# Kernel tuning notes

Hardware: AMD Instinct MI355X
Metric: run time of the kernel (lower is better)

The kernel has to match this reference:

```python
import jax, jax.numpy as jnp
import numpy as np

D = 1024          # d_input_feature
GCN_OUTS = [1024, 512, 256]
DEC_OUTS = [512, 1024, 1024]  # reversed[1:] + [d_input_feature]
EPS = 1e-3        # keras LayerNormalization default epsilon


def _ln(x, gamma, beta):
    m = jnp.mean(x, axis=-1, keepdims=True)
    v = jnp.mean(jnp.square(x - m), axis=-1, keepdims=True)
    return gamma * (x - m) * jax.lax.rsqrt(v + EPS) + beta


def _gcn(x, A, W, b, act):
    # message passing with dense adjacency: act((A @ x) @ W + b)
    h = jnp.einsum('bij,bjd->bid', A, x)
    return act(h @ W + b)


def setup_inputs() -> dict:
    key = jax.random.key(0)
    ks = jax.random.split(key, 40)
    B, DG, DC, NTT = 16384, 772, 100, 128
    inp = {
        't_1': jax.random.randint(ks[0], (B,), 0, NTT),
        'g_1': jax.random.normal(ks[1], (B, DG), jnp.float32),
        'c_1': jax.random.normal(ks[2], (B, DC), jnp.float32),
        'A_1': jax.random.uniform(ks[3], (B, 3, 3), jnp.float32),
        't_2': jax.random.randint(ks[4], (B,), 0, NTT),
        'g_2': jax.random.normal(ks[5], (B, DG), jnp.float32),
        'c_2': jax.random.normal(ks[6], (B, DC), jnp.float32),
        'A_2': jax.random.uniform(ks[7], (B, 3, 3), jnp.float32),
        'embed': jax.random.normal(ks[8], (NTT, D), jnp.float32) * 0.02,
        'Wt': jax.random.normal(ks[9], (D, D), jnp.float32) / np.sqrt(D),
        'bt': jnp.zeros((D,), jnp.float32),
        'Wg': jax.random.normal(ks[10], (DG, D), jnp.float32) / np.sqrt(DG),
        'bg': jnp.zeros((D,), jnp.float32),
        'Wc': jax.random.normal(ks[11], (DC, D), jnp.float32) / np.sqrt(DC),
        'bc': jnp.zeros((D,), jnp.float32),
        'ln_t_g': jnp.ones((D,), jnp.float32), 'ln_t_b': jnp.zeros((D,), jnp.float32),
        'ln_g_g': jnp.ones((D,), jnp.float32), 'ln_g_b': jnp.zeros((D,), jnp.float32),
        'ln_c_g': jnp.ones((D,), jnp.float32), 'ln_c_b': jnp.zeros((D,), jnp.float32),
    }
    d_in = D
    for i, d_out in enumerate(GCN_OUTS):
        inp[f'enc_W{i}'] = jax.random.normal(ks[12 + i], (d_in, d_out), jnp.float32) / np.sqrt(d_in)
        inp[f'enc_b{i}'] = jnp.zeros((d_out,), jnp.float32)
        d_in = d_out
    for i, d_out in enumerate(DEC_OUTS):
        inp[f'dec_W{i}'] = jax.random.normal(ks[20 + i], (d_in, d_out), jnp.float32) / np.sqrt(d_in)
        inp[f'dec_b{i}'] = jnp.zeros((d_out,), jnp.float32)
        d_in = d_out
    return inp


def _branch(t, g, c, embed, Wt, bt, Wg, bg, Wc, bc,
            ln_t_g, ln_t_b, ln_g_g, ln_g_b, ln_c_g, ln_c_b):
    te = embed[t]                               # [B, D]
    te = jax.nn.relu(te @ Wt + bt)
    ge = jax.nn.relu(g @ Wg + bg)
    ce = jax.nn.relu(c @ Wc + bc)
    te = _ln(te, ln_t_g, ln_t_b)
    ge = _ln(ge, ln_g_g, ln_g_b)
    ce = _ln(ce, ln_c_g, ln_c_b)
    return jnp.stack([te, ge, ce], axis=1)      # [B, 3, D]


def _encoder(X, A, enc):
    x = X
    for W, b in enc:
        x = _gcn(x, A, W, b, jax.nn.relu)
    return x


def _decoder(Z, A, dec):
    x = Z
    for W, b in dec:
        x = _gcn(x, A, W, b, jax.nn.silu)       # swish
    return x


def reference(t_1, g_1, c_1, A_1, t_2, g_2, c_2, A_2,
              embed, Wt, bt, Wg, bg, Wc, bc,
              ln_t_g, ln_t_b, ln_g_g, ln_g_b, ln_c_g, ln_c_b,
              enc_W0, enc_b0, enc_W1, enc_b1, enc_W2, enc_b2,
              dec_W0, dec_b0, dec_W1, dec_b1, dec_W2, dec_b2):
    enc = [(enc_W0, enc_b0), (enc_W1, enc_b1), (enc_W2, enc_b2)]
    dec = [(dec_W0, dec_b0), (dec_W1, dec_b1), (dec_W2, dec_b2)]
    bargs = (embed, Wt, bt, Wg, bg, Wc, bc,
             ln_t_g, ln_t_b, ln_g_g, ln_g_b, ln_c_g, ln_c_b)

    X_1 = _branch(t_1, g_1, c_1, *bargs)
    X_2 = _branch(t_2, g_2, c_2, *bargs)
    Z_1 = _encoder(X_1, A_1, enc)
    Z_2 = _encoder(X_2, A_2, enc)
    Z_loss = jnp.square(Z_1 - Z_2)              # [B, 3, 256]

    # GAE reconstruction path (recomputes X per the original code)
    X_h_1 = _decoder(Z_1, A_1, dec)
    X_h_2 = _decoder(Z_2, A_2, dec)
    X_loss = (jnp.square(X_1 - X_h_1) + jnp.square(X_2 - X_h_2)) / 2.0  # [B, 3, D]
    return Z_loss, X_loss
```

## Files before the change

kernel.cpp:

```cpp
#include <hip/hip_runtime.h>


typedef __attribute__((ext_vector_type(8))) short s16x8;
typedef __attribute__((ext_vector_type(4))) short s16x4;
typedef __attribute__((ext_vector_type(4))) float f32x4;

#define DEV static __device__ __forceinline__

DEV float b2f(ushort u) { return __builtin_bit_cast(float, (unsigned)u << 16); }
DEV ushort f2b(float f) {
  unsigned x = __builtin_bit_cast(unsigned, f);
  unsigned r = x + 0x7fffu + ((x >> 16) & 1u);
  return (ushort)(r >> 16);
}

typedef const __attribute__((address_space(1))) void* gas_ptr;
typedef __attribute__((address_space(3))) void* las_ptr;

template<int ACT>
__global__ __launch_bounds__(512, 2) void gemm256(
    const ushort* __restrict__ A, const ushort* __restrict__ BT,
    const float* __restrict__ bias, ushort* __restrict__ C,
    int M, int N, int K)
{
  __shared__ __align__(16) ushort ldsbuf[65536];
  char* Lb = (char*)ldsbuf;

  const int tid = threadIdx.x, lane = tid & 63, w = tid >> 6;
  const int wm = w >> 2, wn = w & 3;

  const int gx  = gridDim.x;
  const int nwg = gx * gridDim.y;
  const int wid = blockIdx.y * gx + blockIdx.x;
  const int q   = nwg >> 3;
  const int Lw  = (wid & 7) * q + (wid >> 3);
  const int bn  = Lw % gx;
  const int bm  = Lw / gx;

  const ushort* Abase = A  + (size_t)bm * 256 * K;
  const ushort* Bbase = BT + (size_t)bn * 256 * K;
  const int T = K >> 6;

  const int srow = w * 8 + (lane >> 3);
  const int scol = (((lane & 7) ^ (lane >> 3)) << 3);

#define STAGE(buf, m, half, Gb, k0)                                          \
  {                                                                          \
    _Pragma("unroll") for (int _j = 0; _j < 2; ++_j) {                       \
      const ushort* _src = (Gb) + (size_t)((half)*128 + _j*64 + srow) * K    \
                           + (k0) + scol;                                    \
      ushort* _dst = (ushort*)(Lb + ((buf)*2 + (m)) * 32768                  \
                               + ((half)*128 + _j*64 + w*8) * 128);          \
      __builtin_amdgcn_global_load_lds((gas_ptr)_src, (las_ptr)_dst, 16,0,0);\
    }                                                                        \
  }

  const int lr = lane & 15, lk = lane >> 4;

#define READ_A(dst, c, mh)                                                   \
  _Pragma("unroll") for (int _i = 0; _i < 4; ++_i)                           \
    _Pragma("unroll") for (int _kk = 0; _kk < 2; ++_kk) {                    \
      const int _r   = (mh)*128 + wm*64 + _i*16 + lr;                        \
      const int _cbb = _kk*64 + lk*16;                                       \
      dst[_i][_kk] = *(const s16x8*)(Lb + ((c)*2 + 0)*32768 + _r*128         \
                                     + (_cbb ^ ((_r & 7) << 4)));            \
    }
#define READ_B(dst, c, nh)                                                   \
  _Pragma("unroll") for (int _p = 0; _p < 2; ++_p)                           \
    _Pragma("unroll") for (int _kk = 0; _kk < 2; ++_kk) {                    \
      const int _r   = (nh)*128 + wn*32 + _p*16 + lr;                        \
      const int _cbb = _kk*64 + lk*16;                                       \
      dst[_p][_kk] = *(const s16x8*)(Lb + ((c)*2 + 1)*32768 + _r*128         \
                                     + (_cbb ^ ((_r & 7) << 4)));            \
    }

#define MFMA_Q(mh, nh)                                                       \
  _Pragma("unroll") for (int _i = 0; _i < 4; ++_i)                           \
    _Pragma("unroll") for (int _p = 0; _p < 2; ++_p)                         \
      _Pragma("unroll") for (int _kk = 0; _kk < 2; ++_kk)                    \
        acc[(mh)*4 + _i][(nh)*2 + _p] =                                      \
            __builtin_amdgcn_mfma_f32_16x16x32_bf16(                         \
                af[_i][_kk], bf[_p][_kk], acc[(mh)*4 + _i][(nh)*2 + _p],     \
                0, 0, 0);

#define MIDBAR  do { __builtin_amdgcn_s_barrier();                           \
                     asm volatile("s_waitcnt lgkmcnt(0)" ::: "memory");      \
                     __builtin_amdgcn_sched_barrier(0);                      \
                     __builtin_amdgcn_s_setprio(1); } while (0)
#define ENDBAR  do { __builtin_amdgcn_s_setprio(0);                          \
                     __builtin_amdgcn_s_barrier(); } while (0)

  f32x4 acc[8][4];
  #pragma unroll
  for (int i = 0; i < 8; ++i)
    #pragma unroll
    for (int j = 0; j < 4; ++j) acc[i][j] = f32x4{0.f, 0.f, 0.f, 0.f};

  STAGE(0, 0, 0, Abase, 0);
  STAGE(0, 1, 0, Bbase, 0);
  STAGE(0, 1, 1, Bbase, 0);
  STAGE(0, 0, 1, Abase, 0);
  STAGE(1, 0, 0, Abase, 64);
  STAGE(1, 1, 1, Bbase, 64);
  STAGE(1, 0, 1, Abase, 64);
  asm volatile("s_waitcnt vmcnt(6)" ::: "memory");
  __builtin_amdgcn_s_barrier();

  for (int t = 0; t < T; ++t) {
    const int cbuf = t & 1, nbuf = cbuf ^ 1;
    const int k1 = ((t + 1 < T) ? t + 1 : t + 1 - T) * 64;
    const int k2 = ((t + 2 < T) ? t + 2 : t + 2 - T) * 64;
    s16x8 af[4][2], bf[2][2];
    READ_A(af, cbuf, 0);
    READ_B(bf, cbuf, 0);
    STAGE(nbuf, 1, 0, Bbase, k1);
    asm volatile("s_waitcnt lgkmcnt(8)" ::: "memory");
    MIDBAR; MFMA_Q(0, 0); ENDBAR;
    READ_B(bf, cbuf, 1);
    STAGE(cbuf, 0, 0, Abase, k2);
    MIDBAR; MFMA_Q(0, 1); ENDBAR;
    READ_A(af, cbuf, 1);
    STAGE(cbuf, 1, 1, Bbase, k2);
    MIDBAR; MFMA_Q(1, 1); ENDBAR;
    READ_B(bf, cbuf, 0);
    STAGE(cbuf, 0, 1, Abase, k2);
    MIDBAR; MFMA_Q(1, 0);
    __builtin_amdgcn_s_setprio(0);
    asm volatile("s_waitcnt vmcnt(6)" ::: "memory");
    __builtin_amdgcn_s_barrier();
  }

  const int row0 = bm * 256, col0 = bn * 256;
  #pragma unroll
  for (int mi = 0; mi < 8; ++mi) {
    const int row = row0 + (mi >> 2) * 128 + wm * 64 + (mi & 3) * 16 + lk * 4;
    #pragma unroll
    for (int ni = 0; ni < 4; ++ni) {
      const int col = col0 + (ni >> 1) * 128 + wn * 32 + (ni & 1) * 16 + lr;
      const float bv = bias[col];
      #pragma unroll
      for (int r = 0; r < 4; ++r) {
        float v = acc[mi][ni][r] + bv;
        if (ACT == 0) v = fmaxf(v, 0.f);
        else          v = v / (1.f + __expf(-v));
        C[(size_t)(row + r) * N + col] = f2b(v);
      }
    }
  }
#undef STAGE
#undef READ_A
#undef READ_B
#undef MFMA_Q
#undef MIDBAR
#undef ENDBAR
}

template<int ACT>
__global__ __launch_bounds__(256, 2) void gemm128(
    const ushort* __restrict__ A, const ushort* __restrict__ BT,
    const float* __restrict__ bias, ushort* __restrict__ C,
    int M, int N, int K)
{
  __shared__ __align__(16) ushort lds[32768];
  char* Lb = (char*)lds;

  const int tid = threadIdx.x, lane = tid & 63;
  const int w = tid >> 6;
  const int wm = w >> 1, wn = w & 1;

  const int gx  = gridDim.x;
  const int nwg = gx * gridDim.y;
  const int wid = blockIdx.y * gx + blockIdx.x;
  const int q   = nwg >> 3;
  const int Lw  = (wid & 7) * q + (wid >> 3);
  const int bn  = Lw % gx;
  const int bm  = Lw / gx;

  const ushort* Abase = A  + (size_t)bm * 128 * K;
  const ushort* Bbase = BT + (size_t)bn * 128 * K;
  const int T = K >> 6;

  const int srow = tid >> 3;
  const int scol = (((tid & 7) ^ (srow & 7)) << 3);

#define STAGE128(buf, k0)                                                    \
  {                                                                          \
    _Pragma("unroll") for (int _j = 0; _j < 4; ++_j)                         \
      __builtin_amdgcn_global_load_lds(                                      \
          (gas_ptr)(Abase + (size_t)(_j * 32 + srow) * K + (k0) + scol),     \
          (las_ptr)(Lb + (buf) + _j * 4096 + tid * 16), 16, 0, 0);           \
    _Pragma("unroll") for (int _j = 0; _j < 4; ++_j)                         \
      __builtin_amdgcn_global_load_lds(                                      \
          (gas_ptr)(Bbase + (size_t)(_j * 32 + srow) * K + (k0) + scol),     \
          (las_ptr)(Lb + (buf) + 16384 + _j * 4096 + tid * 16), 16, 0, 0);   \
  }

  const int lr = lane & 15, lk = lane >> 4;

  f32x4 acc[4][4];
  #pragma unroll
  for (int f = 0; f < 4; ++f)
    #pragma unroll
    for (int p = 0; p < 4; ++p) acc[f][p] = f32x4{0.f, 0.f, 0.f, 0.f};

  STAGE128(0, 0);
  __syncthreads();

  for (int t = 0; t < T; ++t) {
    const int cb = (t & 1) << 15, nb = cb ^ 32768;
    if (t + 1 < T) STAGE128(nb, (t + 1) << 6);

    s16x8 af[4][2], bf[4][2];
    #pragma unroll
    for (int f = 0; f < 4; ++f)
      #pragma unroll
      for (int kk = 0; kk < 2; ++kk) {
        const int r = wm * 64 + f * 16 + lr;
        af[f][kk] = *(const s16x8*)(Lb + cb + r * 128
                                    + ((kk * 64 + lk * 16) ^ ((r & 7) << 4)));
      }
    #pragma unroll
    for (int p = 0; p < 4; ++p)
      #pragma unroll
      for (int kk = 0; kk < 2; ++kk) {
        const int r = wn * 64 + p * 16 + lr;
        bf[p][kk] = *(const s16x8*)(Lb + cb + 16384 + r * 128
                                    + ((kk * 64 + lk * 16) ^ ((r & 7) << 4)));
      }
    #pragma unroll
    for (int f = 0; f < 4; ++f)
      #pragma unroll
      for (int p = 0; p < 4; ++p)
        #pragma unroll
        for (int kk = 0; kk < 2; ++kk)
          acc[f][p] = __builtin_amdgcn_mfma_f32_16x16x32_bf16(
              af[f][kk], bf[p][kk], acc[f][p], 0, 0, 0);

    __syncthreads();
  }

  const int row0 = bm * 128 + wm * 64;
  const int col0 = bn * 128 + wn * 64;
  #pragma unroll
  for (int f = 0; f < 4; ++f) {
    const int row = row0 + f * 16 + lk * 4;
    #pragma unroll
    for (int p = 0; p < 4; ++p) {
      const int col = col0 + p * 16 + lr;
      const float bv = bias[col];
      #pragma unroll
      for (int r = 0; r < 4; ++r) {
        float v = acc[f][p][r] + bv;
        if (ACT == 0) v = fmaxf(v, 0.f);
        else          v = v / (1.f + __expf(-v));
        C[(size_t)(row + r) * N + col] = f2b(v);
      }
    }
  }
#undef STAGE128
}

__global__ void trans_conv(const float* __restrict__ W, ushort* __restrict__ WT,
                           int K, int N, int Kpad)
{
  __shared__ float tile[32][33];
  const int n0 = blockIdx.x * 32, k0 = blockIdx.y * 32;
  const int tx = threadIdx.x, ty = threadIdx.y;
  #pragma unroll
  for (int r = 0; r < 4; r++) {
    const int k = k0 + ty + r * 8;
    tile[ty + r * 8][tx] = (k < K) ? W[(size_t)k * N + n0 + tx] : 0.f;
  }
  __syncthreads();
  #pragma unroll
  for (int r = 0; r < 4; r++) {
    const int n = n0 + ty + r * 8;
    WT[(size_t)n * Kpad + k0 + tx] = f2b(tile[tx][ty + r * 8]);
  }
}

__global__ void conv_pad(const float* __restrict__ in, ushort* __restrict__ out,
                         int R, int Cin, int Cpad)
{
  const int gid = blockIdx.x * 256 + threadIdx.x;
  if (gid >= R * Cpad) return;
  const int r = gid / Cpad, c = gid - r * Cpad;
  out[gid] = (c < Cin) ? f2b(in[(size_t)r * Cin + c]) : (ushort)0;
}

DEV void ln_row(const ushort* __restrict__ in, const float* __restrict__ gamma,
                const float* __restrict__ beta, ushort* __restrict__ outp,
                int tid, float* red)
{
  s16x4 v = *(const s16x4*)&in[tid * 4];
  const float x0 = b2f((ushort)v[0]), x1 = b2f((ushort)v[1]);
  const float x2 = b2f((ushort)v[2]), x3 = b2f((ushort)v[3]);
  float s = x0 + x1 + x2 + x3;
  float qq = x0 * x0 + x1 * x1 + x2 * x2 + x3 * x3;
  #pragma unroll
  for (int o = 32; o > 0; o >>= 1) { s += __shfl_down(s, o); qq += __shfl_down(qq, o); }
  const int wv = tid >> 6, lane = tid & 63;
  __syncthreads();
  if (lane == 0) { red[wv] = s; red[4 + wv] = qq; }
  __syncthreads();
  s  = red[0] + red[1] + red[2] + red[3];
  qq = red[4] + red[5] + red[6] + red[7];
  const float m   = s * (1.f / 1024.f);
  const float var = qq * (1.f / 1024.f) - m * m;
  const float rs  = rsqrtf(var + 1e-3f);
  const int c = tid * 4;
  s16x4 o;
  o[0] = (short)f2b(gamma[c + 0] * ((x0 - m) * rs) + beta[c + 0]);
  o[1] = (short)f2b(gamma[c + 1] * ((x1 - m) * rs) + beta[c + 1]);
  o[2] = (short)f2b(gamma[c + 2] * ((x2 - m) * rs) + beta[c + 2]);
  o[3] = (short)f2b(gamma[c + 3] * ((x3 - m) * rs) + beta[c + 3]);
  *(s16x4*)&outp[c] = o;
}

__global__ void ln_te(const ushort* __restrict__ in, const float* __restrict__ g,
                      const float* __restrict__ b, ushort* __restrict__ out)
{
  __shared__ float red[8];
  ln_row(in + (size_t)blockIdx.x * 1024, g, b,
         out + (size_t)blockIdx.x * 1024, threadIdx.x, red);
}

__global__ void assembleX(const int* __restrict__ ta, const int* __restrict__ tb,
                          int split, const ushort* __restrict__ tetab,
                          const ushort* __restrict__ ge, const ushort* __restrict__ ce,
                          const float* __restrict__ gG, const float* __restrict__ gB,
                          const float* __restrict__ cG, const float* __restrict__ cB,
                          ushort* __restrict__ X)
{
  __shared__ float red[8];
  const int b = blockIdx.x, tid = threadIdx.x;
  const int tt = (b < split) ? ta[b] : tb[b - split];
  *(s16x4*)&X[(size_t)b * 3072 + tid * 4] =
      *(const s16x4*)&tetab[(size_t)tt * 1024 + tid * 4];
  ln_row(ge + (size_t)b * 1024, gG, gB, X + (size_t)b * 3072 + 1024, tid, red);
  ln_row(ce + (size_t)b * 1024, cG, cB, X + (size_t)b * 3072 + 2048, tid, red);
}

__global__ void mix3(const ushort* __restrict__ x,
                     const float* __restrict__ Aa, const float* __restrict__ Ab2,
                     int split, ushort* __restrict__ out, int d, int lg, int nB)
{
  const int gid = blockIdx.x * 256 + threadIdx.x;
  const int b = gid >> lg;
  if (b >= nB) return;
  const int c8 = (gid & ((1 << lg) - 1)) << 3;
  const ushort* xb = x   + (size_t)b * 3 * d + c8;
  ushort*       ob = out + (size_t)b * 3 * d + c8;
  s16x8 x0 = *(const s16x8*)xb;
  s16x8 x1 = *(const s16x8*)(xb + d);
  s16x8 x2 = *(const s16x8*)(xb + 2 * d);
  float f0[8], f1[8], f2[8];
  #pragma unroll
  for (int e = 0; e < 8; e++) {
    f0[e] = b2f((ushort)x0[e]); f1[e] = b2f((ushort)x1[e]); f2[e] = b2f((ushort)x2[e]);
  }
  const float* Ab = (b < split) ? (Aa + (size_t)b * 9)
                                : (Ab2 + (size_t)(b - split) * 9);
  #pragma unroll
  for (int j = 0; j < 3; j++) {
    const float a0 = Ab[j * 3], a1 = Ab[j * 3 + 1], a2 = Ab[j * 3 + 2];
    s16x8 o;
    #pragma unroll
    for (int e = 0; e < 8; e++)
      o[e] = (short)f2b(a0 * f0[e] + a1 * f1[e] + a2 * f2[e]);
    *(s16x8*)(ob + j * d) = o;
  }
}

__global__ void zloss_k(const ushort* __restrict__ z1, const ushort* __restrict__ z2,
                        float* __restrict__ out, int n8)
{
  const int gid = blockIdx.x * 256 + threadIdx.x;
  if (gid >= n8) return;
  const size_t i = (size_t)gid * 8;
  s16x8 a = *(const s16x8*)&z1[i];
  s16x8 b = *(const s16x8*)&z2[i];
  f32x4 o0, o1;
  #pragma unroll
  for (int e = 0; e < 4; e++) {
    float d0 = b2f((ushort)a[e]) - b2f((ushort)b[e]);
    float d1 = b2f((ushort)a[e + 4]) - b2f((ushort)b[e + 4]);
    o0[e] = d0 * d0; o1[e] = d1 * d1;
  }
  *(f32x4*)&out[i] = o0; *(f32x4*)&out[i + 4] = o1;
}

__global__ void xloss2_k(const ushort* __restrict__ X1, const ushort* __restrict__ Xh1,
                         const ushort* __restrict__ X2, const ushort* __restrict__ Xh2,
                         float* __restrict__ out, int n8)
{
  const int gid = blockIdx.x * 256 + threadIdx.x;
  if (gid >= n8) return;
  const size_t i = (size_t)gid * 8;
  s16x8 a1 = *(const s16x8*)&X1[i];
  s16x8 h1 = *(const s16x8*)&Xh1[i];
  s16x8 a2 = *(const s16x8*)&X2[i];
  s16x8 h2 = *(const s16x8*)&Xh2[i];
  f32x4 o0, o1;
  #pragma unroll
  for (int e = 0; e < 4; e++) {
    float d1a = b2f((ushort)a1[e])     - b2f((ushort)h1[e]);
    float d2a = b2f((ushort)a2[e])     - b2f((ushort)h2[e]);
    float d1b = b2f((ushort)a1[e + 4]) - b2f((ushort)h1[e + 4]);
    float d2b = b2f((ushort)a2[e + 4]) - b2f((ushort)h2[e + 4]);
    o0[e] = 0.5f * (d1a * d1a + d2a * d2a);
    o1[e] = 0.5f * (d1b * d1b + d2b * d2b);
  }
  *(f32x4*)&out[i] = o0; *(f32x4*)&out[i + 4] = o1;
}

extern "C" void kernel_launch(void* const* d_in, const int* in_sizes, int n_in,
                              void* d_out, int out_size, void* d_ws, size_t ws_size,
                              hipStream_t stream)
{
  const int B = 16384, S = 3 * B;
  const int*   t1 = (const int*)d_in[0];
  const float* g1 = (const float*)d_in[1];
  const float* c1 = (const float*)d_in[2];
  const float* A1 = (const float*)d_in[3];
  const int*   t2 = (const int*)d_in[4];
  const float* g2 = (const float*)d_in[5];
  const float* c2 = (const float*)d_in[6];
  const float* A2 = (const float*)d_in[7];
  const float* embed = (const float*)d_in[8];
  const float* Wt = (const float*)d_in[9];  const float* bt = (const float*)d_in[10];
  const float* Wg = (const float*)d_in[11]; const float* bg = (const float*)d_in[12];
  const float* Wc = (const float*)d_in[13]; const float* bc = (const float*)d_in[14];
  const float* lntg = (const float*)d_in[15]; const float* lntb = (const float*)d_in[16];
  const float* lngg = (const float*)d_in[17]; const float* lngb = (const float*)d_in[18];
  const float* lncg = (const float*)d_in[19]; const float* lncb = (const float*)d_in[20];
  const float* eW0 = (const float*)d_in[21]; const float* eb0 = (const float*)d_in[22];
  const float* eW1 = (const float*)d_in[23]; const float* eb1 = (const float*)d_in[24];
  const float* eW2 = (const float*)d_in[25]; const float* eb2 = (const float*)d_in[26];
  const float* dW0 = (const float*)d_in[27]; const float* db0 = (const float*)d_in[28];
  const float* dW1 = (const float*)d_in[29]; const float* db1 = (const float*)d_in[30];
  const float* dW2 = (const float*)d_in[31]; const float* db2 = (const float*)d_in[32];
  float* out = (float*)d_out;
  (void)in_sizes; (void)n_in; (void)out_size;

  char* ws = (char*)d_ws; size_t off = 0;
  auto alloc = [&](size_t bytes) -> void* {
    void* p = ws + off; off += (bytes + 255) & ~(size_t)255; return p;
  };
  ushort* WtT  = (ushort*)alloc((size_t)1024 * 1024 * 2);
  ushort* WgT  = (ushort*)alloc((size_t)1024 * 896 * 2);
  ushort* WcT  = (ushort*)alloc((size_t)1024 * 128 * 2);
  ushort* E0T  = (ushort*)alloc((size_t)1024 * 1024 * 2);
  ushort* E1T  = (ushort*)alloc((size_t)512 * 1024 * 2);
  ushort* E2T  = (ushort*)alloc((size_t)256 * 512 * 2);
  ushort* D0T  = (ushort*)alloc((size_t)512 * 256 * 2);
  ushort* D1T  = (ushort*)alloc((size_t)1024 * 512 * 2);
  ushort* D2T  = (ushort*)alloc((size_t)1024 * 1024 * 2);
  ushort* embB = (ushort*)alloc((size_t)128 * 1024 * 2);
  ushort* teraw= (ushort*)alloc((size_t)128 * 1024 * 2);
  ushort* tetab= (ushort*)alloc((size_t)128 * 1024 * 2);
  const size_t woff = off;

  ushort* G  = (ushort*)alloc((size_t)2 * B * 896 * 2);
  ushort* Cc = (ushort*)alloc((size_t)2 * B * 128 * 2);
  ushort* Z  = (ushort*)alloc((size_t)2 * S * 256 * 2);
  ushort* Xs = (ushort*)alloc((size_t)2 * S * 1024 * 2);
  ushort* b0 = (ushort*)alloc((size_t)2 * S * 1024 * 2);
  ushort* b1 = (ushort*)alloc((size_t)2 * S * 1024 * 2);
  const bool merged = (off <= ws_size);

  ushort *fG[2], *fC[2], *fZ[2], *fX[2], *fb0, *fb1, *fxh;
  if (!merged) {
    off = woff;
    fG[0] = (ushort*)alloc((size_t)B * 896 * 2);
    fG[1] = (ushort*)alloc((size_t)B * 896 * 2);
    fC[0] = (ushort*)alloc((size_t)B * 128 * 2);
    fC[1] = (ushort*)alloc((size_t)B * 128 * 2);
    fZ[0] = (ushort*)alloc((size_t)S * 256 * 2);
    fZ[1] = (ushort*)alloc((size_t)S * 256 * 2);
    fX[0] = (ushort*)alloc((size_t)S * 1024 * 2);
    fX[1] = (ushort*)alloc((size_t)S * 1024 * 2);
    fb0   = (ushort*)alloc((size_t)S * 1024 * 2);
    fb1   = (ushort*)alloc((size_t)S * 1024 * 2);
    fxh   = (ushort*)alloc((size_t)S * 1024 * 2);
  }

  const dim3 TB(32, 8);
  trans_conv<<<dim3(32, 32), TB, 0, stream>>>(Wt,  WtT, 1024, 1024, 1024);
  trans_conv<<<dim3(32, 28), TB, 0, stream>>>(Wg,  WgT,  772, 1024,  896);
  trans_conv<<<dim3(32,  4), TB, 0, stream>>>(Wc,  WcT,  100, 1024,  128);
  trans_conv<<<dim3(32, 32), TB, 0, stream>>>(eW0, E0T, 1024, 1024, 1024);
  trans_conv<<<dim3(16, 32), TB, 0, stream>>>(eW1, E1T, 1024,  512, 1024);
  trans_conv<<<dim3( 8, 16), TB, 0, stream>>>(eW2, E2T,  512,  256,  512);
  trans_conv<<<dim3(16,  8), TB, 0, stream>>>(dW0, D0T,  256,  512,  256);
  trans_conv<<<dim3(32, 16), TB, 0, stream>>>(dW1, D1T,  512, 1024,  512);
  trans_conv<<<dim3(32, 32), TB, 0, stream>>>(dW2, D2T, 1024, 1024, 1024);
  conv_pad<<<512, 256, 0, stream>>>(embed, embB, 128, 1024, 1024);
  gemm128<0><<<dim3(8, 1), 256, 0, stream>>>(embB, WtT, bt, teraw, 128, 1024, 1024);
  ln_te<<<128, 256, 0, stream>>>(teraw, lntg, lntb, tetab);

  const size_t ZLEN = (size_t)S * 256;
  const int n8x = S * 1024 / 8;

  auto pipeline = [&](ushort* Gp, ushort* Cp, const int* ta, const int* tb,
                      const float* Aa, const float* Ab2, int split, int nS,
                      ushort* Xp, ushort* p0, ushort* p1, ushort* Zp, ushort* xh) {
    const int Ms = nS * 3;
    gemm256<0><<<dim3(4, nS / 256), 512, 0, stream>>>(Gp, WgT, bg, p0, nS, 1024, 896);
    gemm128<0><<<dim3(8, nS / 128), 256, 0, stream>>>(Cp, WcT, bc, p1, nS, 1024, 128);
    assembleX<<<nS, 256, 0, stream>>>(ta, tb, split, tetab, p0, p1,
                                      lngg, lngb, lncg, lncb, Xp);
    mix3<<<(nS << 7) / 256, 256, 0, stream>>>(Xp, Aa, Ab2, split, p0, 1024, 7, nS);
    gemm256<0><<<dim3(4, Ms / 256), 512, 0, stream>>>(p0, E0T, eb0, p1, Ms, 1024, 1024);
    mix3<<<(nS << 7) / 256, 256, 0, stream>>>(p1, Aa, Ab2, split, p0, 1024, 7, nS);
    gemm256<0><<<dim3(2, Ms / 256), 512, 0, stream>>>(p0, E1T, eb1, p1, Ms, 512, 1024);
    mix3<<<(nS << 6) / 256, 256, 0, stream>>>(p1, Aa, Ab2, split, p0, 512, 6, nS);
    gemm128<0><<<dim3(2, Ms / 128), 256, 0, stream>>>(p0, E2T, eb2, Zp, Ms, 256, 512);
    mix3<<<(nS << 5) / 256, 256, 0, stream>>>(Zp, Aa, Ab2, split, p0, 256, 5, nS);
    gemm128<1><<<dim3(4, Ms / 128), 256, 0, stream>>>(p0, D0T, db0, p1, Ms, 512, 256);
    mix3<<<(nS << 6) / 256, 256, 0, stream>>>(p1, Aa, Ab2, split, p0, 512, 6, nS);
    gemm256<1><<<dim3(4, Ms / 256), 512, 0, stream>>>(p0, D1T, db1, p1, Ms, 1024, 512);
    mix3<<<(nS << 7) / 256, 256, 0, stream>>>(p1, Aa, Ab2, split, p0, 1024, 7, nS);
    gemm256<1><<<dim3(4, Ms / 256), 512, 0, stream>>>(p0, D2T, db2, xh, Ms, 1024, 1024);
  };

  if (merged) {
    conv_pad<<<(B * 896 + 255) / 256, 256, 0, stream>>>(g1, G, B, 772, 896);
    conv_pad<<<(B * 896 + 255) / 256, 256, 0, stream>>>(g2, G + (size_t)B * 896, B, 772, 896);
    conv_pad<<<B * 128 / 256, 256, 0, stream>>>(c1, Cc, B, 100, 128);
    conv_pad<<<B * 128 / 256, 256, 0, stream>>>(c2, Cc + (size_t)B * 128, B, 100, 128);
    pipeline(G, Cc, t1, t2, A1, A2, B, 2 * B, Xs, b0, b1, Z, b1);
    xloss2_k<<<n8x / 256, 256, 0, stream>>>(
        Xs, b1, Xs + (size_t)S * 1024, b1 + (size_t)S * 1024, out + ZLEN, n8x);
    zloss_k<<<(int)(ZLEN / 8 / 256), 256, 0, stream>>>(Z, Z + ZLEN, out, (int)(ZLEN / 8));
  } else {
    for (int br = 0; br < 2; ++br) {
      conv_pad<<<(B * 896 + 255) / 256, 256, 0, stream>>>(br ? g2 : g1, fG[br], B, 772, 896);
      conv_pad<<<B * 128 / 256, 256, 0, stream>>>(br ? c2 : c1, fC[br], B, 100, 128);
      const int*   t    = br ? t2 : t1;
      const float* Aadj = br ? A2 : A1;
      pipeline(fG[br], fC[br], t, t, Aadj, Aadj, B, B,
               fX[br], fb0, fb1, fZ[br], br ? fb1 : fxh);
    }
    xloss2_k<<<n8x / 256, 256, 0, stream>>>(fX[0], fxh, fX[1], fb1, out + ZLEN, n8x);
    zloss_k<<<(int)(ZLEN / 8 / 256), 256, 0, stream>>>(fZ[0], fZ[1], out, (int)(ZLEN / 8));
  }
}
```

Measured before the change: 1.487 ms.

## Fuse 3x3 adjacency mixing into GEMM A-operand load path

Removes the six standalone mix3 kernels and adds a gemm128m kernel that loads three node rows per output row, applies the per-sample 3x3 adjacency weights in registers, and writes the mixed bf16 tile into LDS before the MFMA loop. This avoids a full write and re-read of each layer's activations through global memory. In exchange, every GEMM now uses 128x128 tiles instead of the larger 256-tile variant for the big layers. The A operand also goes through register loads and VALU math instead of direct global-to-LDS copies, and each A element is re-read by the three row tiles that share a sample.

```diff
diff --git a/kernel.cpp b/kernel.cpp
--- a/kernel.cpp
+++ b/kernel.cpp
@@ -260,6 +260,143 @@
 #undef STAGE128
 }
 
+template<int ACT>
+__global__ __launch_bounds__(256, 2) void gemm128m(
+    const ushort* __restrict__ x,
+    const float* __restrict__ Aa, const float* __restrict__ Ab2, int split,
+    const ushort* __restrict__ BT, const float* __restrict__ bias,
+    ushort* __restrict__ C, int M, int N, int K)
+{
+  __shared__ __align__(16) ushort lds[32768];
+  char* Lb = (char*)lds;
+
+  const int tid = threadIdx.x, lane = tid & 63;
+  const int w = tid >> 6;
+  const int wm = w >> 1, wn = w & 1;
+
+  const int gx  = gridDim.x;
+  const int nwg = gx * gridDim.y;
+  const int wid = blockIdx.y * gx + blockIdx.x;
+  const int q   = nwg >> 3;
+  const int Lw  = (wid & 7) * q + (wid >> 3);
+  const int bn  = Lw % gx;
+  const int bm  = Lw / gx;
+
+  const ushort* Bbase = BT + (size_t)bn * 128 * K;
+  const int T = K >> 6;
+
+  const int srow  = tid >> 3;
+  const int lin8  = (tid & 7) * 8;
+  const int swz16 = ((tid & 7) ^ (srow & 7)) << 4;
+  const int swcol = ((tid & 7) ^ (srow & 7)) << 3;
+
+  const ushort* xrow[4];
+  float av[4][3];
+  #pragma unroll
+  for (int j = 0; j < 4; ++j) {
+    const int g = bm * 128 + j * 32 + srow;
+    const int b = g / 3;
+    const int i = g - 3 * b;
+    const float* ad = (b < split) ? (Aa + (size_t)b * 9 + i * 3)
+                                  : (Ab2 + (size_t)(b - split) * 9 + i * 3);
+    av[j][0] = ad[0]; av[j][1] = ad[1]; av[j][2] = ad[2];
+    xrow[j] = x + (size_t)(3 * b) * K + lin8;
+  }
+
+#define STAGEB_M(buf, k0)                                                    \
+  { _Pragma("unroll") for (int _j = 0; _j < 4; ++_j)                         \
+      __builtin_amdgcn_global_load_lds(                                      \
+          (gas_ptr)(Bbase + (size_t)(_j * 32 + srow) * K + (k0) + swcol),    \
+          (las_ptr)(Lb + (buf) + 16384 + _j * 4096 + tid * 16), 16, 0, 0); }
+
+  s16x8 xr[4][3];
+#define LOADX(k0)                                                            \
+  { _Pragma("unroll") for (int _j = 0; _j < 4; ++_j) {                       \
+      const ushort* _xb = xrow[_j] + (k0);                                   \
+      xr[_j][0] = *(const s16x8*)_xb;                                        \
+      xr[_j][1] = *(const s16x8*)(_xb + K);                                  \
+      xr[_j][2] = *(const s16x8*)(_xb + 2 * K); } }
+
+#define WRITEX(buf)                                                          \
+  { _Pragma("unroll") for (int _j = 0; _j < 4; ++_j) {                       \
+      s16x8 _o;                                                              \
+      _Pragma("unroll") for (int _e = 0; _e < 8; ++_e)                       \
+        _o[_e] = (short)f2b(av[_j][0] * b2f((ushort)xr[_j][0][_e])           \
+                          + av[_j][1] * b2f((ushort)xr[_j][1][_e])           \
+                          + av[_j][2] * b2f((ushort)xr[_j][2][_e]));         \
+      *(s16x8*)(Lb + (buf) + _j * 4096 + srow * 128 + swz16) = _o; } }
+
+  const int lr = lane & 15, lk = lane >> 4;
+
+  f32x4 acc[4][4];
+  #pragma unroll
+  for (int f = 0; f < 4; ++f)
+    #pragma unroll
+    for (int p = 0; p < 4; ++p) acc[f][p] = f32x4{0.f, 0.f, 0.f, 0.f};
+
+  LOADX(0);
+  STAGEB_M(0, 0);
+  WRITEX(0);
+  __syncthreads();
+
+  for (int t = 0; t < T; ++t) {
+    const int cb = (t & 1) << 15, nb = cb ^ 32768;
+    const bool hn = (t + 1 < T);
+    if (hn) { STAGEB_M(nb, (t + 1) << 6); LOADX((t + 1) << 6); }
+
+    s16x8 af[4][2], bf[4][2];
+    #pragma unroll
+    for (int f = 0; f < 4; ++f)
+      #pragma unroll
+      for (int kk = 0; kk < 2; ++kk) {
+        const int r = wm * 64 + f * 16 + lr;
+        af[f][kk] = *(const s16x8*)(Lb + cb + r * 128
+                                    + ((kk * 64 + lk * 16) ^ ((r & 7) << 4)));
+      }
+    #pragma unroll
+    for (int p = 0; p < 4; ++p)
+      #pragma unroll
+      for (int kk = 0; kk < 2; ++kk) {
+        const int r = wn * 64 + p * 16 + lr;
+        bf[p][kk] = *(const s16x8*)(Lb + cb + 16384 + r * 128
+                                    + ((kk * 64 + lk * 16) ^ ((r & 7) << 4)));
+      }
+    #pragma unroll
+    for (int f = 0; f < 4; ++f)
+      #pragma unroll
+      for (int p = 0; p < 4; ++p)
+        #pragma unroll
+        for (int kk = 0; kk < 2; ++kk)
+          acc[f][p] = __builtin_amdgcn_mfma_f32_16x16x32_bf16(
+              af[f][kk], bf[p][kk], acc[f][p], 0, 0, 0);
+
+    if (hn) WRITEX(nb);
+    __syncthreads();
+  }
+
+  const int row0 = bm * 128 + wm * 64;
+  const int col0 = bn * 128 + wn * 64;
+  #pragma unroll
+  for (int f = 0; f < 4; ++f) {
+    const int row = row0 + f * 16 + lk * 4;
+    #pragma unroll
+    for (int p = 0; p < 4; ++p) {
+      const int col = col0 + p * 16 + lr;
+      const float bv = bias[col];
+      #pragma unroll
+      for (int r = 0; r < 4; ++r) {
+        float v = acc[f][p][r] + bv;
+        if (ACT == 0) v = fmaxf(v, 0.f);
+        else          v = v / (1.f + __expf(-v));
+        C[(size_t)(row + r) * N + col] = f2b(v);
+      }
+    }
+  }
+#undef STAGEB_M
+#undef LOADX
+#undef WRITEX
+}
+
 __global__ void trans_conv(const float* __restrict__ W, ushort* __restrict__ WT,
                            int K, int N, int Kpad)
 {
@@ -339,37 +476,6 @@
       *(const s16x4*)&tetab[(size_t)tt * 1024 + tid * 4];
   ln_row(ge + (size_t)b * 1024, gG, gB, X + (size_t)b * 3072 + 1024, tid, red);
   ln_row(ce + (size_t)b * 1024, cG, cB, X + (size_t)b * 3072 + 2048, tid, red);
-}
-
-__global__ void mix3(const ushort* __restrict__ x,
-                     const float* __restrict__ Aa, const float* __restrict__ Ab2,
-                     int split, ushort* __restrict__ out, int d, int lg, int nB)
-{
-  const int gid = blockIdx.x * 256 + threadIdx.x;
-  const int b = gid >> lg;
-  if (b >= nB) return;
-  const int c8 = (gid & ((1 << lg) - 1)) << 3;
-  const ushort* xb = x   + (size_t)b * 3 * d + c8;
-  ushort*       ob = out + (size_t)b * 3 * d + c8;
-  s16x8 x0 = *(const s16x8*)xb;
-  s16x8 x1 = *(const s16x8*)(xb + d);
-  s16x8 x2 = *(const s16x8*)(xb + 2 * d);
-  float f0[8], f1[8], f2[8];
-  #pragma unroll
-  for (int e = 0; e < 8; e++) {
-    f0[e] = b2f((ushort)x0[e]); f1[e] = b2f((ushort)x1[e]); f2[e] = b2f((ushort)x2[e]);
-  }
-  const float* Ab = (b < split) ? (Aa + (size_t)b * 9)
-                                : (Ab2 + (size_t)(b - split) * 9);
-  #pragma unroll
-  for (int j = 0; j < 3; j++) {
-    const float a0 = Ab[j * 3], a1 = Ab[j * 3 + 1], a2 = Ab[j * 3 + 2];
-    s16x8 o;
-    #pragma unroll
-    for (int e = 0; e < 8; e++)
-      o[e] = (short)f2b(a0 * f0[e] + a1 * f1[e] + a2 * f2[e]);
-    *(s16x8*)(ob + j * d) = o;
-  }
 }
 
 __global__ void zloss_k(const ushort* __restrict__ z1, const ushort* __restrict__ z2,
@@ -510,18 +616,12 @@
     gemm128<0><<<dim3(8, nS / 128), 256, 0, stream>>>(Cp, WcT, bc, p1, nS, 1024, 128);
     assembleX<<<nS, 256, 0, stream>>>(ta, tb, split, tetab, p0, p1,
                                       lngg, lngb, lncg, lncb, Xp);
-    mix3<<<(nS << 7) / 256, 256, 0, stream>>>(Xp, Aa, Ab2, split, p0, 1024, 7, nS);
-    gemm256<0><<<dim3(4, Ms / 256), 512, 0, stream>>>(p0, E0T, eb0, p1, Ms, 1024, 1024);
-    mix3<<<(nS << 7) / 256, 256, 0, stream>>>(p1, Aa, Ab2, split, p0, 1024, 7, nS);
-    gemm256<0><<<dim3(2, Ms / 256), 512, 0, stream>>>(p0, E1T, eb1, p1, Ms, 512, 1024);
-    mix3<<<(nS << 6) / 256, 256, 0, stream>>>(p1, Aa, Ab2, split, p0, 512, 6, nS);
-    gemm128<0><<<dim3(2, Ms / 128), 256, 0, stream>>>(p0, E2T, eb2, Zp, Ms, 256, 512);
-    mix3<<<(nS << 5) / 256, 256, 0, stream>>>(Zp, Aa, Ab2, split, p0, 256, 5, nS);
-    gemm128<1><<<dim3(4, Ms / 128), 256, 0, stream>>>(p0, D0T, db0, p1, Ms, 512, 256);
-    mix3<<<(nS << 6) / 256, 256, 0, stream>>>(p1, Aa, Ab2, split, p0, 512, 6, nS);
-    gemm256<1><<<dim3(4, Ms / 256), 512, 0, stream>>>(p0, D1T, db1, p1, Ms, 1024, 512);
-    mix3<<<(nS << 7) / 256, 256, 0, stream>>>(p1, Aa, Ab2, split, p0, 1024, 7, nS);
-    gemm256<1><<<dim3(4, Ms / 256), 512, 0, stream>>>(p0, D2T, db2, xh, Ms, 1024, 1024);
+    gemm128m<0><<<dim3(8, Ms / 128), 256, 0, stream>>>(Xp, Aa, Ab2, split, E0T, eb0, p1, Ms, 1024, 1024);
+    gemm128m<0><<<dim3(4, Ms / 128), 256, 0, stream>>>(p1, Aa, Ab2, split, E1T, eb1, p0, Ms, 512, 1024);
+    gemm128m<0><<<dim3(2, Ms / 128), 256, 0, stream>>>(p0, Aa, Ab2, split, E2T, eb2, Zp, Ms, 256, 512);
+    gemm128m<1><<<dim3(4, Ms / 128), 256, 0, stream>>>(Zp, Aa, Ab2, split, D0T, db0, p1, Ms, 512, 256);
+    gemm128m<1><<<dim3(8, Ms / 128), 256, 0, stream>>>(p1, Aa, Ab2, split, D1T, db1, p0, Ms, 1024, 512);
+    gemm128m<1><<<dim3(8, Ms / 128), 256, 0, stream>>>(p0, Aa, Ab2, split, D2T, db2, xh, Ms, 1024, 1024);
   };
 
   if (merged) {
```

After: 1.860 ms. +25.1%, slower.

## Reorder encoder layers to apply weights before adjacency mix, batch prep kernels

Applied to the files above, without the earlier changes.

For encoder layers 1 and 2, the GEMM now runs first on the unmixed input with no bias or activation, and a new mixact kernel then applies the 3x3 adjacency mix, bias and ReLU. This uses associativity (A·X)·W = A·(X·W), so the mix works on the narrower output width (512 or 256) instead of the wider input. The nine weight-transpose launches are merged into one 3D-grid kernel, and the five input convert/pad launches into one grid-stride kernel, to cut launch overhead. Rounding to bf16 now happens at a different point, which slightly changes the numerics.

```diff
diff --git a/kernel.cpp b/kernel.cpp
--- a/kernel.cpp
+++ b/kernel.cpp
@@ -137,12 +137,12 @@
     #pragma unroll
     for (int ni = 0; ni < 4; ++ni) {
       const int col = col0 + (ni >> 1) * 128 + wn * 32 + (ni & 1) * 16 + lr;
-      const float bv = bias[col];
+      const float bv = (ACT == 2) ? 0.f : bias[col];
       #pragma unroll
       for (int r = 0; r < 4; ++r) {
         float v = acc[mi][ni][r] + bv;
-        if (ACT == 0) v = fmaxf(v, 0.f);
-        else          v = v / (1.f + __expf(-v));
+        if (ACT == 0)      v = fmaxf(v, 0.f);
+        else if (ACT == 1) v = v / (1.f + __expf(-v));
         C[(size_t)(row + r) * N + col] = f2b(v);
       }
     }
@@ -247,12 +247,12 @@
     #pragma unroll
     for (int p = 0; p < 4; ++p) {
       const int col = col0 + p * 16 + lr;
-      const float bv = bias[col];
+      const float bv = (ACT == 2) ? 0.f : bias[col];
       #pragma unroll
       for (int r = 0; r < 4; ++r) {
         float v = acc[f][p][r] + bv;
-        if (ACT == 0) v = fmaxf(v, 0.f);
-        else          v = v / (1.f + __expf(-v));
+        if (ACT == 0)      v = fmaxf(v, 0.f);
+        else if (ACT == 1) v = v / (1.f + __expf(-v));
         C[(size_t)(row + r) * N + col] = f2b(v);
       }
     }
@@ -260,32 +260,45 @@
 #undef STAGE128
 }
 
-__global__ void trans_conv(const float* __restrict__ W, ushort* __restrict__ WT,
-                           int K, int N, int Kpad)
+struct TP { const float* W; ushort* WT; int K, N, Kpad; };
+struct TP9 { TP t[9]; };
+
+__global__ void trans_all(TP9 ps)
 {
   __shared__ float tile[32][33];
+  const TP tp = ps.t[blockIdx.z];
   const int n0 = blockIdx.x * 32, k0 = blockIdx.y * 32;
+  if (n0 >= tp.N || k0 >= tp.Kpad) return;
   const int tx = threadIdx.x, ty = threadIdx.y;
   #pragma unroll
   for (int r = 0; r < 4; r++) {
     const int k = k0 + ty + r * 8;
-    tile[ty + r * 8][tx] = (k < K) ? W[(size_t)k * N + n0 + tx] : 0.f;
+    tile[ty + r * 8][tx] = (k < tp.K) ? tp.W[(size_t)k * tp.N + n0 + tx] : 0.f;
   }
   __syncthreads();
   #pragma unroll
   for (int r = 0; r < 4; r++) {
     const int n = n0 + ty + r * 8;
-    WT[(size_t)n * Kpad + k0 + tx] = f2b(tile[tx][ty + r * 8]);
-  }
-}
-
-__global__ void conv_pad(const float* __restrict__ in, ushort* __restrict__ out,
-                         int R, int Cin, int Cpad)
-{
-  const int gid = blockIdx.x * 256 + threadIdx.x;
-  if (gid >= R * Cpad) return;
-  const int r = gid / Cpad, c = gid - r * Cpad;
-  out[gid] = (c < Cin) ? f2b(in[(size_t)r * Cin + c]) : (ushort)0;
+    tp.WT[(size_t)n * tp.Kpad + k0 + tx] = f2b(tile[tx][ty + r * 8]);
+  }
+}
+
+struct CP { const float* in; ushort* out; int Cin, Cpad; size_t total; };
+struct CP5 { CP s[5]; size_t cum[5]; };
+
+__global__ void conv_all(CP5 ps, size_t grand)
+{
+  for (size_t gid = (size_t)blockIdx.x * 256 + threadIdx.x; gid < grand;
+       gid += (size_t)gridDim.x * 256) {
+    int si = 0;
+    #pragma unroll
+    for (int k = 1; k < 5; ++k) si += (gid >= ps.cum[k - 1]);
+    const CP sp = ps.s[si];
+    const size_t l = gid - (si ? ps.cum[si - 1] : 0);
+    const size_t r = l / sp.Cpad;
+    const int c = (int)(l - r * sp.Cpad);
+    sp.out[l] = (c < sp.Cin) ? f2b(sp.in[r * sp.Cin + c]) : (ushort)0;
+  }
 }
 
 DEV void ln_row(const ushort* __restrict__ in, const float* __restrict__ gamma,
@@ -368,6 +381,42 @@
     #pragma unroll
     for (int e = 0; e < 8; e++)
       o[e] = (short)f2b(a0 * f0[e] + a1 * f1[e] + a2 * f2[e]);
+    *(s16x8*)(ob + j * d) = o;
+  }
+}
+
+__global__ void mixact(const ushort* __restrict__ y,
+                       const float* __restrict__ Aa, const float* __restrict__ Ab2,
+                       int split, const float* __restrict__ bias,
+                       ushort* __restrict__ out, int d, int lg, int nB)
+{
+  const int gid = blockIdx.x * 256 + threadIdx.x;
+  const int b = gid >> lg;
+  if (b >= nB) return;
+  const int c8 = (gid & ((1 << lg) - 1)) << 3;
+  const ushort* yb = y   + (size_t)b * 3 * d + c8;
+  ushort*       ob = out + (size_t)b * 3 * d + c8;
+  s16x8 y0 = *(const s16x8*)yb;
+  s16x8 y1 = *(const s16x8*)(yb + d);
+  s16x8 y2 = *(const s16x8*)(yb + 2 * d);
+  f32x4 bv0 = *(const f32x4*)&bias[c8];
+  f32x4 bv1 = *(const f32x4*)&bias[c8 + 4];
+  float f0[8], f1[8], f2[8];
+  #pragma unroll
+  for (int e = 0; e < 8; e++) {
+    f0[e] = b2f((ushort)y0[e]); f1[e] = b2f((ushort)y1[e]); f2[e] = b2f((ushort)y2[e]);
+  }
+  const float* Ab = (b < split) ? (Aa + (size_t)b * 9)
+                                : (Ab2 + (size_t)(b - split) * 9);
+  #pragma unroll
+  for (int j = 0; j < 3; j++) {
+    const float a0 = Ab[j * 3], a1 = Ab[j * 3 + 1], a2 = Ab[j * 3 + 2];
+    s16x8 o;
+    #pragma unroll
+    for (int e = 0; e < 8; e++) {
+      const float bb = (e < 4) ? bv0[e] : bv1[e - 4];
+      o[e] = (short)f2b(fmaxf(a0 * f0[e] + a1 * f1[e] + a2 * f2[e] + bb, 0.f));
+    }
     *(s16x8*)(ob + j * d) = o;
   }
 }
@@ -485,17 +534,42 @@
     fxh   = (ushort*)alloc((size_t)S * 1024 * 2);
   }
 
-  const dim3 TB(32, 8);
-  trans_conv<<<dim3(32, 32), TB, 0, stream>>>(Wt,  WtT, 1024, 1024, 1024);
-  trans_conv<<<dim3(32, 28), TB, 0, stream>>>(Wg,  WgT,  772, 1024,  896);
-  trans_conv<<<dim3(32,  4), TB, 0, stream>>>(Wc,  WcT,  100, 1024,  128);
-  trans_conv<<<dim3(32, 32), TB, 0, stream>>>(eW0, E0T, 1024, 1024, 1024);
-  trans_conv<<<dim3(16, 32), TB, 0, stream>>>(eW1, E1T, 1024,  512, 1024);
-  trans_conv<<<dim3( 8, 16), TB, 0, stream>>>(eW2, E2T,  512,  256,  512);
-  trans_conv<<<dim3(16,  8), TB, 0, stream>>>(dW0, D0T,  256,  512,  256);
-  trans_conv<<<dim3(32, 16), TB, 0, stream>>>(dW1, D1T,  512, 1024,  512);
-  trans_conv<<<dim3(32, 32), TB, 0, stream>>>(dW2, D2T, 1024, 1024, 1024);
-  conv_pad<<<512, 256, 0, stream>>>(embed, embB, 128, 1024, 1024);
+  TP9 tp;
+  tp.t[0] = {Wt,  WtT, 1024, 1024, 1024};
+  tp.t[1] = {Wg,  WgT,  772, 1024,  896};
+  tp.t[2] = {Wc,  WcT,  100, 1024,  128};
+  tp.t[3] = {eW0, E0T, 1024, 1024, 1024};
+  tp.t[4] = {eW1, E1T, 1024,  512, 1024};
+  tp.t[5] = {eW2, E2T,  512,  256,  512};
+  tp.t[6] = {dW0, D0T,  256,  512,  256};
+  tp.t[7] = {dW1, D1T,  512, 1024,  512};
+  tp.t[8] = {dW2, D2T, 1024, 1024, 1024};
+  trans_all<<<dim3(32, 32, 9), dim3(32, 8), 0, stream>>>(tp);
+
+  {
+    CP5 cp;
+    const float* srcs[5] = {embed, g1, g2, c1, c2};
+    ushort* dsts[5];
+    int cins[5]  = {1024, 772, 772, 100, 100};
+    int cpads[5] = {1024, 896, 896, 128, 128};
+    int rs[5]    = {128, B, B, B, B};
+    if (merged) {
+      dsts[0] = embB; dsts[1] = G; dsts[2] = G + (size_t)B * 896;
+      dsts[3] = Cc;   dsts[4] = Cc + (size_t)B * 128;
+    } else {
+      dsts[0] = embB; dsts[1] = fG[0]; dsts[2] = fG[1];
+      dsts[3] = fC[0]; dsts[4] = fC[1];
+    }
+    size_t cum = 0;
+    for (int i = 0; i < 5; ++i) {
+      cp.s[i] = {srcs[i], dsts[i], cins[i], cpads[i],
+                 (size_t)rs[i] * cpads[i]};
+      cum += cp.s[i].total; cp.cum[i] = cum;
+    }
+    const int grid = 2048;
+    conv_all<<<grid, 256, 0, stream>>>(cp, cum);
+  }
+
   gemm128<0><<<dim3(8, 1), 256, 0, stream>>>(embB, WtT, bt, teraw, 128, 1024, 1024);
   ln_te<<<128, 256, 0, stream>>>(teraw, lntg, lntb, tetab);
 
@@ -512,10 +586,10 @@
                                       lngg, lngb, lncg, lncb, Xp);
     mix3<<<(nS << 7) / 256, 256, 0, stream>>>(Xp, Aa, Ab2, split, p0, 1024, 7, nS);
     gemm256<0><<<dim3(4, Ms / 256), 512, 0, stream>>>(p0, E0T, eb0, p1, Ms, 1024, 1024);
-    mix3<<<(nS << 7) / 256, 256, 0, stream>>>(p1, Aa, Ab2, split, p0, 1024, 7, nS);
-    gemm256<0><<<dim3(2, Ms / 256), 512, 0, stream>>>(p0, E1T, eb1, p1, Ms, 512, 1024);
-    mix3<<<(nS << 6) / 256, 256, 0, stream>>>(p1, Aa, Ab2, split, p0, 512, 6, nS);
-    gemm128<0><<<dim3(2, Ms / 128), 256, 0, stream>>>(p0, E2T, eb2, Zp, Ms, 256, 512);
+    gemm256<2><<<dim3(2, Ms / 256), 512, 0, stream>>>(p1, E1T, nullptr, p0, Ms, 512, 1024);
+    mixact<<<(nS << 6) / 256, 256, 0, stream>>>(p0, Aa, Ab2, split, eb1, p1, 512, 6, nS);
+    gemm128<2><<<dim3(2, Ms / 128), 256, 0, stream>>>(p1, E2T, nullptr, p0, Ms, 256, 512);
+    mixact<<<(nS << 5) / 256, 256, 0, stream>>>(p0, Aa, Ab2, split, eb2, Zp, 256, 5, nS);
     mix3<<<(nS << 5) / 256, 256, 0, stream>>>(Zp, Aa, Ab2, split, p0, 256, 5, nS);
     gemm128<1><<<dim3(4, Ms / 128), 256, 0, stream>>>(p0, D0T, db0, p1, Ms, 512, 256);
     mix3<<<(nS << 6) / 256, 256, 0, stream>>>(p1, Aa, Ab2, split, p0, 512, 6, nS);
@@ -525,18 +599,12 @@
   };
 
   if (merged) {
-    conv_pad<<<(B * 896 + 255) / 256, 256, 0, stream>>>(g1, G, B, 772, 896);
-    conv_pad<<<(B * 896 + 255) / 256, 256, 0, stream>>>(g2, G + (size_t)B * 896, B, 772, 896);
-    conv_pad<<<B * 128 / 256, 256, 0, stream>>>(c1, Cc, B, 100, 128);
-    conv_pad<<<B * 128 / 256, 256, 0, stream>>>(c2, Cc + (size_t)B * 128, B, 100, 128);
     pipeline(G, Cc, t1, t2, A1, A2, B, 2 * B, Xs, b0, b1, Z, b1);
     xloss2_k<<<n8x / 256, 256, 0, stream>>>(
         Xs, b1, Xs + (size_t)S * 1024, b1 + (size_t)S * 1024, out + ZLEN, n8x);
     zloss_k<<<(int)(ZLEN / 8 / 256), 256, 0, stream>>>(Z, Z + ZLEN, out, (int)(ZLEN / 8));
   } else {
     for (int br = 0; br < 2; ++br) {
-      conv_pad<<<(B * 896 + 255) / 256, 256, 0, stream>>>(br ? g2 : g1, fG[br], B, 772, 896);
-      conv_pad<<<B * 128 / 256, 256, 0, stream>>>(br ? c2 : c1, fC[br], B, 100, 128);
       const int*   t    = br ? t2 : t1;
       const float* Aadj = br ? A2 : A1;
       pipeline(fG[br], fC[br], t, t, Aadj, Aadj, B, B,
```

After: 1.422 ms. 1.05x faster.
